# Kernel tuning notes

Measured on AMD Instinct MI355X. Metric: run time of the kernel, lower is better.

## Reference

```python
import jax, jax.numpy as jnp
import numpy as np

N_NODES = 50000
N_EDGES = 800000
D = 128
N_LAYERS = 4


def _sage_conv(x, edge_index, Wl, bl, Wr):
    # PyG SAGEConv (mean aggr): out = lin_l(mean_{j in N(i)} x_j) + lin_r(x_i)
    src, dst = edge_index[0], edge_index[1]
    msgs = x[src]                                            # [E, D] gather
    summed = jax.ops.segment_sum(msgs, dst, num_segments=N_NODES)   # [N, D]
    cnt = jax.ops.segment_sum(jnp.ones((msgs.shape[0],), x.dtype), dst,
                              num_segments=N_NODES)
    mean = summed / jnp.maximum(cnt, 1.0)[:, None]           # [N, D]
    return mean @ Wl.T + bl + x @ Wr.T


def setup_inputs() -> dict:
    key = jax.random.key(0)
    ks = jax.random.split(key, 2 + 3 * N_LAYERS)
    x = jax.random.normal(ks[0], (N_NODES, D), dtype=jnp.float32)
    edge_index = jax.random.randint(ks[1], (2, N_EDGES), 0, N_NODES, dtype=jnp.int64)
    inp = {"x": x, "edge_index": edge_index}
    s = 1.0 / np.sqrt(D)
    for i in range(N_LAYERS):
        inp[f"Wl{i}"] = jax.random.uniform(ks[2 + 3 * i], (D, D), jnp.float32, -s, s)
        inp[f"bl{i}"] = jax.random.uniform(ks[3 + 3 * i], (D,), jnp.float32, -s, s)
        inp[f"Wr{i}"] = jax.random.uniform(ks[4 + 3 * i], (D, D), jnp.float32, -s, s)
    return inp


def reference(x, edge_index, Wl0, bl0, Wr0, Wl1, bl1, Wr1, Wl2, bl2, Wr2, Wl3, bl3, Wr3):
    # ReLU only after the first conv, per the original forward.
    h = jax.nn.relu(_sage_conv(x, edge_index, Wl0, bl0, Wr0))
    h = _sage_conv(h, edge_index, Wl1, bl1, Wr1)
    h = _sage_conv(h, edge_index, Wl2, bl2, Wr2)
    h = _sage_conv(h, edge_index, Wl3, bl3, Wr3)
    return h
```

## Files before the change

kernel.cpp:

```cpp
#include <hip/hip_runtime.h>
#include <stdint.h>

#define NN 50000
#define NE 800000
#define NB 196

typedef short short8 __attribute__((ext_vector_type(8)));
typedef float f32x4 __attribute__((ext_vector_type(4)));
typedef unsigned int uint;
typedef unsigned short ushort;

__device__ __forceinline__ uint rne_bf16(float f) {
    uint x = __float_as_uint(f);
    return (x + 0x7FFFu + ((x >> 16) & 1u)) >> 16;
}
__device__ __forceinline__ float bf_lo(uint d) { return __uint_as_float(d << 16); }
__device__ __forceinline__ float bf_hi(uint d) { return __uint_as_float(d & 0xFFFF0000u); }

__global__ void k_detect(const int* __restrict__ ei, int* __restrict__ flag) {
    int l = threadIdx.x;
    int v = (l < 16) ? ei[2 * l + 1] : 0;
    unsigned long long nz = __ballot(v != 0);
    if (l == 0 && blockIdx.x == 0) *flag = (nz == 0ULL) ? 1 : 0;
}

__global__ void k_count(const int* __restrict__ ei, const int* __restrict__ flag,
                        int* __restrict__ deg, ushort* __restrict__ rank) {
    int e = blockIdx.x * 256 + threadIdx.x;
    if (e >= NE) return;
    int is64 = *flag;
    int d = is64 ? ei[2 * NE + 2 * e] : ei[NE + e];
    int rk = atomicAdd(&deg[d], 1);
    rank[e] = (ushort)rk;
}

__global__ __launch_bounds__(256) void k_blocksum(const int* __restrict__ deg,
                                                  int* __restrict__ bsum) {
    __shared__ int s[256];
    int i = blockIdx.x * 256 + threadIdx.x;
    s[threadIdx.x] = (i < NN) ? deg[i] : 0;
    __syncthreads();
    for (int off = 128; off > 0; off >>= 1) {
        if (threadIdx.x < off) s[threadIdx.x] += s[threadIdx.x + off];
        __syncthreads();
    }
    if (threadIdx.x == 0) bsum[blockIdx.x] = s[0];
}

__global__ __launch_bounds__(256) void k_scanb(const int* __restrict__ bsum,
                                               int* __restrict__ boff) {
    __shared__ int s[256];
    int t = threadIdx.x;
    s[t] = (t < NB) ? bsum[t] : 0;
    __syncthreads();
    for (int off = 1; off < 256; off <<= 1) {
        int v = s[t];
        int a = (t >= off) ? s[t - off] : 0;
        __syncthreads();
        s[t] = v + a;
        __syncthreads();
    }
    if (t < NB) boff[t] = (t == 0) ? 0 : s[t - 1];
}

__global__ __launch_bounds__(256) void k_writeptr(const int* __restrict__ deg,
                                                  const int* __restrict__ boff,
                                                  int* __restrict__ row_ptr,
                                                  float* __restrict__ rinv) {
    __shared__ int s[256];
    int b = blockIdx.x, t = threadIdx.x;
    int i = b * 256 + t;
    int d = (i < NN) ? deg[i] : 0;
    s[t] = d;
    __syncthreads();
    for (int off = 1; off < 256; off <<= 1) {
        int v = s[t];
        int a = (t >= off) ? s[t - off] : 0;
        __syncthreads();
        s[t] = v + a;
        __syncthreads();
    }
    if (i < NN) {
        int pos = boff[b] + s[t] - d;
        row_ptr[i] = pos;
        rinv[i] = 1.0f / (float)max(d, 1);
    }
    if (b == 0 && t == 0) row_ptr[NN] = NE;
}

__global__ void k_fill(const int* __restrict__ ei, const int* __restrict__ flag,
                       const int* __restrict__ row_ptr,
                       const ushort* __restrict__ rank, ushort* __restrict__ col) {
    int e = blockIdx.x * 256 + threadIdx.x;
    if (e >= NE) return;
    int is64 = *flag;
    int sv = is64 ? ei[2 * e] : ei[e];
    int dv = is64 ? ei[2 * NE + 2 * e] : ei[NE + e];
    int p = row_ptr[dv] + (int)rank[e];
    col[p] = (ushort)sv;
}

__global__ __launch_bounds__(256) void k_cast_x(const float* __restrict__ x,
                                                ushort* __restrict__ xbf) {
    int i = blockIdx.x * 256 + threadIdx.x;
    float4 v = ((const float4*)x)[i];
    uint2 o;
    o.x = rne_bf16(v.x) | (rne_bf16(v.y) << 16);
    o.y = rne_bf16(v.z) | (rne_bf16(v.w) << 16);
    ((uint2*)xbf)[i] = o;
}

struct Ptrs8 { const float* p[8]; };
__global__ __launch_bounds__(256) void k_cvtW(Ptrs8 ps, ushort* __restrict__ wbf) {
    int idx = blockIdx.x * 256 + threadIdx.x;
    int m = idx >> 14;
    int off = idx & 16383;
    wbf[idx] = (ushort)rne_bf16(ps.p[m][off]);
}

__global__ __launch_bounds__(256) void k_agg3(const ushort* __restrict__ h,
                                              const int* __restrict__ row_ptr,
                                              const ushort* __restrict__ col,
                                              const float* __restrict__ rinv,
                                              ushort* __restrict__ mean) {
    int node = blockIdx.x * 4 + (threadIdx.x >> 6);
    if (node >= NN) return;
    int lane = threadIdx.x & 63;
    int beg = row_ptr[node], end = row_ptr[node + 1];
    const uint* hp = (const uint*)h;
    float a0 = 0.f, a1 = 0.f;
    for (int b = beg; b < end; b += 64) {
        int n = min(64, end - b);
        int c = (int)col[b + min(lane, n - 1)];
        for (int j0 = 0; j0 < n; j0 += 8) {
#pragma unroll
            for (int j = 0; j < 8; j++) {
                int jj = j0 + j;
                int s = __shfl(c, min(jj, n - 1));
                uint v = hp[s * 64 + lane];
                float m = (jj < n) ? 1.f : 0.f;
                a0 = fmaf(m, bf_lo(v), a0);
                a1 = fmaf(m, bf_hi(v), a1);
            }
        }
    }
    float r = rinv[node];
    ((uint*)mean)[node * 64 + lane] = rne_bf16(a0 * r) | (rne_bf16(a1 * r) << 16);
}

__global__ __launch_bounds__(256) void k_gemm_mfma(
    const ushort* __restrict__ Am, const ushort* __restrict__ Ah,
    const ushort* __restrict__ Wlb, const ushort* __restrict__ Wrb,
    const float* __restrict__ bias, float* __restrict__ outf,
    ushort* __restrict__ outb, int relu) {
    const int lane = threadIdx.x & 63;
    const int wave = threadIdx.x >> 6;
    const int l15 = lane & 15;
    const int quad = lane >> 4;
    const int m0 = blockIdx.x * 64 + wave * 16;

    f32x4 acc[8];
#pragma unroll
    for (int t = 0; t < 8; t++) acc[t] = (f32x4){0.f, 0.f, 0.f, 0.f};

    int arow = min(m0 + l15, NN - 1);
    const ushort* Arm = Am + (size_t)arow * 128 + quad * 8;
    const ushort* Arh = Ah + (size_t)arow * 128 + quad * 8;
    const int wro = quad * 8;

#pragma unroll
    for (int half = 0; half < 2; half++) {
        const ushort* Ar = half ? Arh : Arm;
        const ushort* W = half ? Wrb : Wlb;
#pragma unroll
        for (int k0 = 0; k0 < 128; k0 += 32) {
            short8 a = *(const short8*)(Ar + k0);
#pragma unroll
            for (int t = 0; t < 8; t++) {
                short8 b = *(const short8*)(W + (size_t)(t * 16 + l15) * 128 + k0 + wro);
                acc[t] = __builtin_amdgcn_mfma_f32_16x16x32_bf16(a, b, acc[t], 0, 0, 0);
            }
        }
    }

    float bb[8];
#pragma unroll
    for (int t = 0; t < 8; t++) bb[t] = bias[t * 16 + l15];

#pragma unroll
    for (int r = 0; r < 4; r++) {
        int row = m0 + quad * 4 + r;
        if (row < NN) {
#pragma unroll
            for (int t = 0; t < 8; t++) {
                float v = acc[t][r] + bb[t];
                if (relu) v = fmaxf(v, 0.f);
                if (outb) outb[(size_t)row * 128 + t * 16 + l15] = (ushort)rne_bf16(v);
                else outf[(size_t)row * 128 + t * 16 + l15] = v;
            }
        }
    }
}

extern "C" void kernel_launch(void* const* d_in, const int* in_sizes, int n_in,
                              void* d_out, int out_size, void* d_ws, size_t ws_size,
                              hipStream_t stream) {
    const float* x = (const float*)d_in[0];
    const int* ei = (const int*)d_in[1];
    const float* Wl[4] = {(const float*)d_in[2], (const float*)d_in[5],
                          (const float*)d_in[8], (const float*)d_in[11]};
    const float* bl[4] = {(const float*)d_in[3], (const float*)d_in[6],
                          (const float*)d_in[9], (const float*)d_in[12]};
    const float* Wr[4] = {(const float*)d_in[4], (const float*)d_in[7],
                          (const float*)d_in[10], (const float*)d_in[13]};
    float* out = (float*)d_out;

    char* p = (char*)d_ws;
    auto take = [&](size_t bytes) -> char* {
        char* r = p;
        p += (bytes + 255) & ~(size_t)255;
        return r;
    };
    int* flag = (int*)take(4);
    int* deg = (int*)take(NN * 4);
    int* row_ptr = (int*)take((NN + 1) * 4);
    float* rinv = (float*)take(NN * 4);
    int* bsum = (int*)take(NB * 4);
    int* boff = (int*)take(NB * 4);
    ushort* rank = (ushort*)take((size_t)NE * 2);
    ushort* col = (ushort*)take((size_t)NE * 2 + 256);
    ushort* xbf = (ushort*)take((size_t)NN * 128 * 2);
    ushort* h1 = (ushort*)take((size_t)NN * 128 * 2);
    ushort* h2 = (ushort*)take((size_t)NN * 128 * 2);
    ushort* meanbf = (ushort*)take((size_t)NN * 128 * 2);
    ushort* wbf = (ushort*)take(8 * 16384 * 2);

    hipMemsetAsync(deg, 0, NN * 4, stream);
    k_detect<<<1, 64, 0, stream>>>(ei, flag);
    k_count<<<(NE + 255) / 256, 256, 0, stream>>>(ei, flag, deg, rank);
    k_blocksum<<<NB, 256, 0, stream>>>(deg, bsum);
    k_scanb<<<1, 256, 0, stream>>>(bsum, boff);
    k_writeptr<<<NB, 256, 0, stream>>>(deg, boff, row_ptr, rinv);
    k_fill<<<(NE + 255) / 256, 256, 0, stream>>>(ei, flag, row_ptr, rank, col);

    k_cast_x<<<(NN * 128 / 4) / 256, 256, 0, stream>>>(x, xbf);
    Ptrs8 ps;
    ps.p[0] = Wl[0]; ps.p[1] = Wr[0]; ps.p[2] = Wl[1]; ps.p[3] = Wr[1];
    ps.p[4] = Wl[2]; ps.p[5] = Wr[2]; ps.p[6] = Wl[3]; ps.p[7] = Wr[3];
    k_cvtW<<<512, 256, 0, stream>>>(ps, wbf);

    const ushort* h = xbf;
    ushort* houts[4] = {h1, h2, h1, nullptr};
    for (int l = 0; l < 4; l++) {
        k_agg3<<<(NN + 3) / 4, 256, 0, stream>>>(h, row_ptr, col, rinv, meanbf);
        k_gemm_mfma<<<(NN + 63) / 64, 256, 0, stream>>>(
            meanbf, h, wbf + (size_t)(2 * l) * 16384,
            wbf + (size_t)(2 * l + 1) * 16384, bl[l], out, houts[l],
            l == 0 ? 1 : 0);
        h = houts[l];
    }
}
```

Measured before the change: 426.4 us.

## Replace global-atomic CSR build with chunked LDS histograms and column scan

The CSR construction no longer uses global atomics on per-node degree counters. Edges are split into 128 chunks and destinations into 4 ranges, and each block builds a local histogram in LDS with shared-memory atomics. A column scan then produces per-chunk offsets and degrees, and a second pass fills col using LDS-atomic ranks. This removes global atomic contention and the memset, at the cost of two extra 12.8MB intermediate arrays, each edge chunk being read four times, and a strided column-scan kernel.

Measured after the change: 425.2 us. No clear change (-0.3%).

```diff
diff --git a/kernel.cpp b/kernel.cpp
--- a/kernel.cpp
+++ b/kernel.cpp
@@ -4,6 +4,10 @@
 #define NN 50000
 #define NE 800000
 #define NB 196
+#define NCH 128
+#define CHSZ 6250
+#define NR 4
+#define RSZ 16384
 
 typedef short short8 __attribute__((ext_vector_type(8)));
 typedef float f32x4 __attribute__((ext_vector_type(4)));
@@ -24,14 +28,39 @@
     if (l == 0 && blockIdx.x == 0) *flag = (nz == 0ULL) ? 1 : 0;
 }
 
-__global__ void k_count(const int* __restrict__ ei, const int* __restrict__ flag,
-                        int* __restrict__ deg, ushort* __restrict__ rank) {
-    int e = blockIdx.x * 256 + threadIdx.x;
-    if (e >= NE) return;
+__global__ __launch_bounds__(256) void k_hist(const int* __restrict__ ei,
+                                              const int* __restrict__ flag,
+                                              ushort* __restrict__ hist) {
+    __shared__ uint lh[RSZ];
+    int c = blockIdx.x >> 2;
+    int d0 = (blockIdx.x & 3) * RSZ;
+    for (int i = threadIdx.x; i < RSZ; i += 256) lh[i] = 0;
+    __syncthreads();
     int is64 = *flag;
-    int d = is64 ? ei[2 * NE + 2 * e] : ei[NE + e];
-    int rk = atomicAdd(&deg[d], 1);
-    rank[e] = (ushort)rk;
+    int base = c * CHSZ;
+    for (int i = threadIdx.x; i < CHSZ; i += 256) {
+        int e = base + i;
+        int dv = is64 ? ei[2 * NE + 2 * e] : ei[NE + e];
+        int rel = dv - d0;
+        if ((unsigned)rel < RSZ) atomicAdd(&lh[rel], 1u);
+    }
+    __syncthreads();
+    int lim = min(RSZ, NN - d0);
+    for (int i = threadIdx.x; i < lim; i += 256)
+        hist[(size_t)c * NN + d0 + i] = (ushort)lh[i];
+}
+
+__global__ __launch_bounds__(256) void k_colscan(const ushort* __restrict__ hist,
+                                                 ushort* __restrict__ coff,
+                                                 int* __restrict__ deg) {
+    int d = blockIdx.x * 256 + threadIdx.x;
+    if (d >= NN) return;
+    int run = 0;
+    for (int c = 0; c < NCH; c++) {
+        coff[(size_t)c * NN + d] = (ushort)run;
+        run += hist[(size_t)c * NN + d];
+    }
+    deg[d] = run;
 }
 
 __global__ __launch_bounds__(256) void k_blocksum(const int* __restrict__ deg,
@@ -88,16 +117,29 @@
     if (b == 0 && t == 0) row_ptr[NN] = NE;
 }
 
-__global__ void k_fill(const int* __restrict__ ei, const int* __restrict__ flag,
-                       const int* __restrict__ row_ptr,
-                       const ushort* __restrict__ rank, ushort* __restrict__ col) {
-    int e = blockIdx.x * 256 + threadIdx.x;
-    if (e >= NE) return;
+__global__ __launch_bounds__(256) void k_fill2(const int* __restrict__ ei,
+                                               const int* __restrict__ flag,
+                                               const int* __restrict__ row_ptr,
+                                               const ushort* __restrict__ coff,
+                                               ushort* __restrict__ col) {
+    __shared__ uint lh[RSZ];
+    int c = blockIdx.x >> 2;
+    int d0 = (blockIdx.x & 3) * RSZ;
+    for (int i = threadIdx.x; i < RSZ; i += 256) lh[i] = 0;
+    __syncthreads();
     int is64 = *flag;
-    int sv = is64 ? ei[2 * e] : ei[e];
-    int dv = is64 ? ei[2 * NE + 2 * e] : ei[NE + e];
-    int p = row_ptr[dv] + (int)rank[e];
-    col[p] = (ushort)sv;
+    int base = c * CHSZ;
+    for (int i = threadIdx.x; i < CHSZ; i += 256) {
+        int e = base + i;
+        int dv = is64 ? ei[2 * NE + 2 * e] : ei[NE + e];
+        int rel = dv - d0;
+        if ((unsigned)rel < RSZ) {
+            int sv = is64 ? ei[2 * e] : ei[e];
+            uint lrk = atomicAdd(&lh[rel], 1u);
+            int p = row_ptr[dv] + (int)coff[(size_t)c * NN + dv] + (int)lrk;
+            col[p] = (ushort)sv;
+        }
+    }
 }
 
 __global__ __launch_bounds__(256) void k_cast_x(const float* __restrict__ x,
@@ -227,7 +269,8 @@
     float* rinv = (float*)take(NN * 4);
     int* bsum = (int*)take(NB * 4);
     int* boff = (int*)take(NB * 4);
-    ushort* rank = (ushort*)take((size_t)NE * 2);
+    ushort* hist = (ushort*)take((size_t)NCH * NN * 2);
+    ushort* coff = (ushort*)take((size_t)NCH * NN * 2);
     ushort* col = (ushort*)take((size_t)NE * 2 + 256);
     ushort* xbf = (ushort*)take((size_t)NN * 128 * 2);
     ushort* h1 = (ushort*)take((size_t)NN * 128 * 2);
@@ -235,13 +278,13 @@
     ushort* meanbf = (ushort*)take((size_t)NN * 128 * 2);
     ushort* wbf = (ushort*)take(8 * 16384 * 2);
 
-    hipMemsetAsync(deg, 0, NN * 4, stream);
     k_detect<<<1, 64, 0, stream>>>(ei, flag);
-    k_count<<<(NE + 255) / 256, 256, 0, stream>>>(ei, flag, deg, rank);
+    k_hist<<<NCH * NR, 256, 0, stream>>>(ei, flag, hist);
+    k_colscan<<<NB, 256, 0, stream>>>(hist, coff, deg);
     k_blocksum<<<NB, 256, 0, stream>>>(deg, bsum);
     k_scanb<<<1, 256, 0, stream>>>(bsum, boff);
     k_writeptr<<<NB, 256, 0, stream>>>(deg, boff, row_ptr, rinv);
-    k_fill<<<(NE + 255) / 256, 256, 0, stream>>>(ei, flag, row_ptr, rank, col);
+    k_fill2<<<NCH * NR, 256, 0, stream>>>(ei, flag, row_ptr, coff, col);
 
     k_cast_x<<<(NN * 128 / 4) / 256, 256, 0, stream>>>(x, xbf);
     Ptrs8 ps;
```
